# Kernel tuning notes

Measured on AMD Instinct MI355X. Metric: run time of the kernel, lower is better.

Reference implementation:

```python
import jax, jax.numpy as jnp
import numpy as np

B, N, C, H = 2, 2048, 768, 12
D = C // H
SCALE = D ** -0.5
STEP = 0.1
LAMBD = 0.5
EPS = 1e-12  # F.normalize eps


def setup_inputs() -> dict:
    key = jax.random.key(0)
    k1, k2, k3 = jax.random.split(key, 3)
    x = jax.random.normal(k1, (B, N, C), dtype=jnp.float32)
    Wqkv = jax.random.normal(k2, (3 * C, C), dtype=jnp.float32) * 0.02
    Wproj = jax.random.normal(k3, (C, C), dtype=jnp.float32) * 0.02
    bproj = jnp.zeros((C,), dtype=jnp.float32)
    return {"x": x, "Wqkv": Wqkv, "Wproj": Wproj, "bproj": bproj}


def _l2_normalize(t):
    # matches F.normalize(t, dim=-1): t / max(||t||_2, eps)
    n = jnp.sqrt(jnp.sum(t * t, axis=-1, keepdims=True))
    return t / jnp.maximum(n, EPS)


def reference(x, Wqkv, Wproj, bproj):
    b, n, c = x.shape
    # qkv: [B,N,3C] -> [3,B,H,N,D]
    qkv = (x @ Wqkv.T).reshape(b, n, 3, H, D).transpose(2, 0, 3, 1, 4)
    q, k, v = qkv[0], qkv[1], qkv[2]
    q = _l2_normalize(q)
    k = _l2_normalize(k)
    attn = jnp.einsum('bhnd,bhmd->bhnm', q, k) * SCALE
    x1 = jnp.einsum('bhnm,bhmd->bhnd', attn, v)        # weight @ x
    grad_1 = jnp.einsum('bhnm,bhnd->bhmd', attn, x1)   # weight^T @ x1
    grad_2 = jnp.einsum('bhnm,bhnd->bhmd', attn, v)    # weight^T @ x
    grad_update = STEP * (grad_2 - grad_1) - STEP * LAMBD
    out = jax.nn.relu(v + grad_update)                 # [B,H,N,D]
    out = out.transpose(0, 2, 1, 3).reshape(b, n, c)   # [B,N,C]
    return out @ Wproj.T + bproj
```

## Files before the change

### kernel.cpp

```cpp
#include <hip/hip_runtime.h>
#include <hip/hip_bf16.h>

typedef __attribute__((ext_vector_type(8))) __bf16 bf16x8;
typedef __attribute__((ext_vector_type(4))) float f32x4;

#define HBF __hip_bfloat16

static constexpr float SCALE_C = 0.125f;
static constexpr float STEP_C  = 0.1f;
static constexpr float LAMBD_C = 0.5f;

__device__ __forceinline__ int sane_f(float v) {
    float a = fabsf(v);
    return (a <= 1.0e4f && (a >= 1.0e-6f || v == 0.0f)) ? 1 : 0;
}

__global__ __launch_bounds__(256) void convert_all(const void* __restrict__ x,
                                                   const void* __restrict__ wqkv,
                                                   const void* __restrict__ wproj,
                                                   const void* __restrict__ bproj,
                                                   HBF* __restrict__ xb,
                                                   HBF* __restrict__ wqkvb,
                                                   HBF* __restrict__ wprojb,
                                                   HBF* __restrict__ bprojb,
                                                   int* __restrict__ flag) {
    const int t = threadIdx.x, lane = t & 63;
    const unsigned int w = ((const unsigned int*)x)[lane];
    const float f  = __uint_as_float(w);
    const float h0 = __uint_as_float((w & 0xFFFFu) << 16);
    const float h1 = __uint_as_float(w & 0xFFFF0000u);
    int s32 = sane_f(f);
    int s16 = sane_f(h0) + sane_f(h1);
#pragma unroll
    for (int off = 32; off >= 1; off >>= 1) {
        s32 += __shfl_xor(s32, off, 64);
        s16 += __shfl_xor(s16, off, 64);
    }
    const int isf32 = (2 * s32 >= s16) ? 1 : 0;
    if (blockIdx.x == 0 && t == 0) flag[0] = isf32;

    constexpr int C0 = (4096 * 768) / 8;
    constexpr int C1 = C0 + (2304 * 768) / 8;
    constexpr int C2 = C1 + (768 * 768) / 8;
    constexpr int C3 = C2 + 768 / 8;

    int i = blockIdx.x * 256 + t;
    const int stride = gridDim.x * 256;
    for (; i < C3; i += stride) {
        const void* src; HBF* dst; int e;
        if (i < C0)      { src = x;     dst = xb;     e = i; }
        else if (i < C1) { src = wqkv;  dst = wqkvb;  e = i - C0; }
        else if (i < C2) { src = wproj; dst = wprojb; e = i - C1; }
        else             { src = bproj; dst = bprojb; e = i - C2; }
        if (isf32) {
            const float4* s = (const float4*)src;
            float4 a = s[2 * e], b = s[2 * e + 1];
            HBF o[8] = {__float2bfloat16(a.x), __float2bfloat16(a.y),
                        __float2bfloat16(a.z), __float2bfloat16(a.w),
                        __float2bfloat16(b.x), __float2bfloat16(b.y),
                        __float2bfloat16(b.z), __float2bfloat16(b.w)};
            ((uint4*)dst)[e] = *(const uint4*)o;
        } else {
            ((uint4*)dst)[e] = ((const uint4*)src)[e];
        }
    }
}

template <int NJ, bool BIAS, bool FINAL, bool SPLITQKV>
__global__ __launch_bounds__(256) void gemm128(const HBF* __restrict__ A,
                                               const HBF* __restrict__ B,
                                               const HBF* __restrict__ bias,
                                               void* __restrict__ Cout,
                                               HBF* __restrict__ knat,
                                               HBF* __restrict__ vnat,
                                               HBF* __restrict__ tbuf,
                                               int M, int N, int K,
                                               const int* __restrict__ flagp) {
    constexpr int TN = NJ * 32;
    __shared__ HBF smem[128 * 64 + TN * 64];
    HBF* As = smem;
    HBF* Bs = smem + 128 * 64;

    int outf32 = 0;
    if (FINAL) outf32 = *flagp;

    const int tid  = threadIdx.x;
    const int wv   = tid >> 6, lane = tid & 63;
    const int m0   = blockIdx.x * 128, n0 = blockIdx.y * TN;
    const int wr = wv >> 1, wc = wv & 1;
    const int l15 = lane & 15, quad = lane >> 4;
    const int srow   = lane >> 3;
    const int schunk = (lane & 7) ^ srow;

    f32x4 acc[4][NJ] = {};

    for (int k0 = 0; k0 < K; k0 += 64) {
#pragma unroll
        for (int d = 0; d < 4; d++) {
            const int region = d * 4 + wv;
            const int row = region * 8 + srow;
            const HBF* ga = A + (size_t)(m0 + row) * K + k0 + schunk * 8;
            __builtin_amdgcn_global_load_lds((const void*)ga, (void*)(As + region * 512), 16, 0, 0);
        }
#pragma unroll
        for (int d = 0; d < TN / 32; d++) {
            const int region = d * 4 + wv;
            const int row = region * 8 + srow;
            const HBF* gb = B + (size_t)(n0 + row) * K + k0 + schunk * 8;
            __builtin_amdgcn_global_load_lds((const void*)gb, (void*)(Bs + region * 512), 16, 0, 0);
        }
        __syncthreads();

#pragma unroll
        for (int s = 0; s < 2; s++) {
            bf16x8 af[4], bfr[NJ];
#pragma unroll
            for (int i = 0; i < 4; i++) {
                const int row = wr * 64 + i * 16 + l15;
                const int ch = (s * 4 + quad) ^ (row & 7);
                af[i] = *reinterpret_cast<const bf16x8*>(&As[row * 64 + ch * 8]);
            }
#pragma unroll
            for (int j = 0; j < NJ; j++) {
                const int col = wc * (NJ * 16) + j * 16 + l15;
                const int ch = (s * 4 + quad) ^ (col & 7);
                bfr[j] = *reinterpret_cast<const bf16x8*>(&Bs[col * 64 + ch * 8]);
            }
#pragma unroll
            for (int i = 0; i < 4; i++)
#pragma unroll
                for (int j = 0; j < NJ; j++)
                    acc[i][j] = __builtin_amdgcn_mfma_f32_16x16x32_bf16(af[i], bfr[j], acc[i][j], 0, 0, 0);
        }
        __syncthreads();
    }

    if (SPLITQKV) {
        HBF* wpriv = smem + wv * 4096;
        const int colbase = n0 + wc * 64;
        const int tsel = (colbase >= 1536) ? 2 : (colbase >= 768 ? 1 : 0);
        const int h = (colbase - tsel * 768) >> 6;

        if (tsel < 2) {
#pragma unroll
            for (int i = 0; i < 4; i++)
#pragma unroll
                for (int r = 0; r < 4; r++) {
                    float ss = acc[i][0][r] * acc[i][0][r] + acc[i][1][r] * acc[i][1][r]
                             + acc[i][2][r] * acc[i][2][r] + acc[i][3][r] * acc[i][3][r];
#pragma unroll
                    for (int off = 1; off <= 8; off <<= 1) ss += __shfl_xor(ss, off, 64);
                    const float inv = 1.0f / fmaxf(sqrtf(ss), 1e-12f);
#pragma unroll
                    for (int j = 0; j < 4; j++) acc[i][j][r] *= inv;
                }
        }

#pragma unroll
        for (int ih = 0; ih < 2; ih++) {
            const int rowstart = m0 + wr * 64 + ih * 32;
            const int b = rowstart >> 11, nloc = rowstart & 2047;
            const size_t bh = (size_t)(b * 12 + h);

            if (tsel != 0) {
                HBF* ep = wpriv;
#pragma unroll
                for (int ii = 0; ii < 2; ii++) {
                    const int i = ih * 2 + ii;
#pragma unroll
                    for (int j = 0; j < 4; j++)
#pragma unroll
                        for (int r = 0; r < 4; r++)
                            ep[(ii * 16 + quad * 4 + r) * 72 + j * 16 + l15] =
                                __float2bfloat16(acc[i][j][r]);
                }
                HBF* dst0 = ((tsel == 2) ? vnat : knat) + (bh * 2048 + nloc) * 64;
#pragma unroll
                for (int it = 0; it < 4; it++) {
                    const int idx = it * 64 + lane;
                    const int rl = idx >> 3, ch = idx & 7;
                    const uint4 val = *(const uint4*)((const char*)ep + rl * 144 + ch * 16);
                    *(uint4*)((char*)dst0 + rl * 128 + ch * 16) = val;
                }
            }
            {
                HBF* epT = wpriv;
#pragma unroll
                for (int ii = 0; ii < 2; ii++) {
                    const int i = ih * 2 + ii;
#pragma unroll
                    for (int j = 0; j < 4; j++)
#pragma unroll
                        for (int r = 0; r < 4; r++)
                            epT[(j * 16 + l15) * 34 + ii * 16 + quad * 4 + r] =
                                __float2bfloat16(acc[i][j][r]);
                }
                HBF* tdst = tbuf + (size_t)tsel * (24 * 64 * 2048) + (bh * 64) * 2048 + nloc;
#pragma unroll
                for (int it = 0; it < 4; it++) {
                    const int idx = it * 64 + lane;
                    const int d = idx >> 2, c = idx & 3;
                    const uint4 val = *(const uint4*)(epT + d * 34 + c * 8);
                    *(uint4*)(tdst + (size_t)d * 2048 + c * 8) = val;
                }
            }
        }
        return;
    }

    float bvals[NJ];
#pragma unroll
    for (int j = 0; j < NJ; j++) {
        bvals[j] = 0.f;
        if (BIAS) bvals[j] = __bfloat162float(bias[n0 + wc * NJ * 16 + j * 16 + l15]);
    }

    if (FINAL && outf32) {
#pragma unroll
        for (int i = 0; i < 4; i++)
#pragma unroll
            for (int j = 0; j < NJ; j++) {
                const int col = n0 + wc * NJ * 16 + j * 16 + l15;
#pragma unroll
                for (int r = 0; r < 4; r++) {
                    const int row = m0 + wr * 64 + i * 16 + quad * 4 + r;
                    ((float*)Cout)[(size_t)row * N + col] = acc[i][j][r] + bvals[j];
                }
            }
        return;
    }

    constexpr int RS = (NJ == 4) ? 72 : 40;
    constexpr int CH = NJ * 2;
    constexpr int ITERS = 32 * CH / 64;
    HBF* ep = smem + wv * (32 * RS);

#pragma unroll
    for (int ih = 0; ih < 2; ih++) {
#pragma unroll
        for (int ii = 0; ii < 2; ii++) {
            const int i = ih * 2 + ii;
#pragma unroll
            for (int j = 0; j < NJ; j++)
#pragma unroll
                for (int r = 0; r < 4; r++)
                    ep[(ii * 16 + quad * 4 + r) * RS + j * 16 + l15] =
                        __float2bfloat16(acc[i][j][r] + bvals[j]);
        }
        const int rowstart = m0 + wr * 64 + ih * 32;
#pragma unroll
        for (int it = 0; it < ITERS; it++) {
            const int idx = it * 64 + lane;
            const int rl = idx / CH, ch = idx % CH;
            const uint4 val = *(const uint4*)((const char*)ep + rl * (RS * 2) + ch * 16);
            const int grow = rowstart + rl;
            const int col = n0 + wc * NJ * 16 + ch * 8;
            *(uint4*)((HBF*)Cout + (size_t)grow * N + col) = val;
        }
    }
}

__global__ __launch_bounds__(256) void gram_mfma(const HBF* __restrict__ QKVt,
                                                 float* __restrict__ P) {
    __shared__ HBF lds[3 * 8192];
    const int bh = blockIdx.x, cn = blockIdx.y;
    const int t = threadIdx.x, wv = t >> 6, lane = t & 63;
    const int l15 = lane & 15, quad = lane >> 4;
    constexpr size_t S = (size_t)24 * 64 * 2048;
    const HBF* srcs[3] = {QKVt + S, QKVt, QKVt + 2 * S};

    const int rowq = lane >> 4;
    const int cgb  = lane & 15;
#pragma unroll
    for (int t3 = 0; t3 < 3; t3++) {
        const HBF* base = srcs[t3] + (size_t)bh * 64 * 2048 + cn * 128;
#pragma unroll
        for (int rg = 0; rg < 4; rg++) {
            const int region = rg * 4 + wv;
            const int row = region * 4 + rowq;
            const int cg = cgb ^ (row & 15);
            __builtin_amdgcn_global_load_lds((const void*)(base + (size_t)row * 2048 + cg * 8),
                                             (void*)(lds + t3 * 8192 + region * 512), 16, 0, 0);
        }
    }
    __syncthreads();

    const HBF* Kt = lds;
    const HBF* Qt = lds + 8192;
    const HBF* Vt = lds + 16384;
    f32x4 aKV[4] = {}, aQV[4] = {}, aQQ[4] = {};
    const int i = wv;
#pragma unroll
    for (int s = 0; s < 4; s++) {
        const int q = (s * 4 + quad) ^ l15;
        const bf16x8 aK = *(const bf16x8*)(Kt + (i * 16 + l15) * 128 + q * 8);
        const bf16x8 aQ = *(const bf16x8*)(Qt + (i * 16 + l15) * 128 + q * 8);
#pragma unroll
        for (int j = 0; j < 4; j++) {
            const bf16x8 bV = *(const bf16x8*)(Vt + (j * 16 + l15) * 128 + q * 8);
            const bf16x8 bQ = *(const bf16x8*)(Qt + (j * 16 + l15) * 128 + q * 8);
            aKV[j] = __builtin_amdgcn_mfma_f32_16x16x32_bf16(aK, bV, aKV[j], 0, 0, 0);
            aQV[j] = __builtin_amdgcn_mfma_f32_16x16x32_bf16(aQ, bV, aQV[j], 0, 0, 0);
            aQQ[j] = __builtin_amdgcn_mfma_f32_16x16x32_bf16(aQ, bQ, aQQ[j], 0, 0, 0);
        }
    }

    float* Pb = P + ((size_t)bh * 16 + cn) * 12288;
#pragma unroll
    for (int j = 0; j < 4; j++)
#pragma unroll
        for (int r = 0; r < 4; r++) {
            const int row = i * 16 + quad * 4 + r, col = j * 16 + l15;
            Pb[row * 64 + col]        = aKV[j][r];
            Pb[4096 + row * 64 + col] = aQV[j][r];
            Pb[8192 + row * 64 + col] = aQQ[j][r];
        }
}

__global__ __launch_bounds__(256) void gram_reduce(const float* __restrict__ P,
                                                   float* __restrict__ M) {
    const int o = blockIdx.x * 256 + threadIdx.x;
    const int head = o / 12288, e = o % 12288;
    const float* Pb = P + (size_t)head * 16 * 12288 + e;
    float s = 0.f;
#pragma unroll
    for (int k = 0; k < 16; k++) s += Pb[(size_t)k * 12288];
    M[o] = s;
}

__global__ __launch_bounds__(256) void combine_w(const float* __restrict__ M,
                                                 HBF* __restrict__ Wt) {
    const int bh = blockIdx.x;
    const int by = blockIdx.y;
    const int t = threadIdx.x;
    __shared__ float Kv[4096];
    __shared__ float Qq8[512];
    const float* Mb = M + (size_t)bh * 12288;
#pragma unroll
    for (int r = 0; r < 16; r++) Kv[t + 256 * r] = Mb[t + 256 * r];
#pragma unroll
    for (int r = 0; r < 2; r++)  Qq8[t + 256 * r] = Mb[8192 + by * 512 + t + 256 * r];
    __syncthreads();

    const int il = t >> 5;
    const int j0 = (t & 31) * 2;
    float s0 = 0.f, s1 = 0.f;
#pragma unroll
    for (int k = 0; k < 64; k++) {
        const float q = Qq8[il * 64 + k];
        const float2 kv = *(const float2*)&Kv[k * 64 + j0];
        s0 += q * kv.x;
        s1 += q * kv.y;
    }
    const int i = by * 8 + il;
    const float w0 = STEP_C * (SCALE_C * Mb[4096 + i * 64 + j0]     - SCALE_C * SCALE_C * s0);
    const float w1 = STEP_C * (SCALE_C * Mb[4096 + i * 64 + j0 + 1] - SCALE_C * SCALE_C * s1);
    Wt[(size_t)bh * 4096 + j0 * 64 + i]       = __float2bfloat16(w0);
    Wt[(size_t)bh * 4096 + (j0 + 1) * 64 + i] = __float2bfloat16(w1);
}

__global__ __launch_bounds__(256) void epilogue_attn(const HBF* __restrict__ Kn,
                                                     const HBF* __restrict__ Vb,
                                                     const HBF* __restrict__ Wt,
                                                     HBF* __restrict__ AO) {
    __shared__ char smem[34816];
    HBF* Ks  = (HBF*)smem;
    HBF* Wts = Ks + 128 * 64;
    float* Ps = (float*)smem;

    const int bh = blockIdx.x, cn = blockIdx.y;
    const int b = bh / 12, h = bh % 12;
    const int t = threadIdx.x, wv = t >> 6, lane = t & 63;
    const int l15 = lane & 15, quad = lane >> 4;
    const size_t kbase = ((size_t)bh * 2048 + cn * 128) * 64;
    const int srow = lane >> 3;
    const int schunk = (lane & 7) ^ srow;
    const int sub = t & 7;

#pragma unroll
    for (int rg = 0; rg < 4; rg++) {
        const int region = rg * 4 + wv;
        const int row = region * 8 + srow;
        __builtin_amdgcn_global_load_lds((const void*)(Kn + kbase + (size_t)row * 64 + schunk * 8),
                                         (void*)(Ks + region * 512), 16, 0, 0);
    }
#pragma unroll
    for (int rg = 0; rg < 2; rg++) {
        const int region = rg * 4 + wv;
        const int row = region * 8 + srow;
        __builtin_amdgcn_global_load_lds((const void*)(Wt + (size_t)bh * 4096 + (size_t)row * 64 + schunk * 8),
                                         (void*)(Wts + region * 512), 16, 0, 0);
    }
    __syncthreads();

    f32x4 acc[2][4] = {};
#pragma unroll
    for (int s = 0; s < 2; s++) {
        const int ch = (s * 4 + quad) ^ (l15 & 7);
        bf16x8 af[2], bfr[4];
#pragma unroll
        for (int i = 0; i < 2; i++) {
            const int row = wv * 32 + i * 16 + l15;
            af[i] = *reinterpret_cast<const bf16x8*>(&Ks[row * 64 + ch * 8]);
        }
#pragma unroll
        for (int j = 0; j < 4; j++) {
            const int d = j * 16 + l15;
            bfr[j] = *reinterpret_cast<const bf16x8*>(&Wts[d * 64 + ch * 8]);
        }
#pragma unroll
        for (int i = 0; i < 2; i++)
#pragma unroll
            for (int j = 0; j < 4; j++)
                acc[i][j] = __builtin_amdgcn_mfma_f32_16x16x32_bf16(af[i], bfr[j], acc[i][j], 0, 0, 0);
    }
    __syncthreads();

    float* Pw = Ps + wv * (32 * 68);
#pragma unroll
    for (int i = 0; i < 2; i++)
#pragma unroll
        for (int j = 0; j < 4; j++)
#pragma unroll
            for (int r = 0; r < 4; r++)
                Pw[(i * 16 + quad * 4 + r) * 68 + j * 16 + l15] = acc[i][j][r];
    __syncthreads();

#pragma unroll
    for (int rr = 0; rr < 4; rr++) {
        const int row = rr * 32 + (t >> 3);
        const float* prow = Ps + (row >> 5) * (32 * 68) + (row & 31) * 68 + sub * 8;
        const float4 p0 = *(const float4*)prow;
        const float4 p1 = *(const float4*)(prow + 4);
        uint4 rv = *(const uint4*)(Vb + kbase + (size_t)row * 64 + sub * 8);
        const HBF* hv = (const HBF*)&rv;
        const float pv[8] = {p0.x, p0.y, p0.z, p0.w, p1.x, p1.y, p1.z, p1.w};
        HBF o[8];
#pragma unroll
        for (int i = 0; i < 8; i++)
            o[i] = __float2bfloat16(fmaxf(__bfloat162float(hv[i]) + pv[i] - (STEP_C * LAMBD_C), 0.f));
        const int n = cn * 128 + row;
        *(uint4*)(AO + ((size_t)b * 2048 + n) * 768 + h * 64 + sub * 8) = *(const uint4*)o;
    }
}

extern "C" void kernel_launch(void* const* d_in, const int* in_sizes, int n_in,
                              void* d_out, int out_size, void* d_ws, size_t ws_size,
                              hipStream_t stream) {
    char* ws = (char*)d_ws;
    size_t off = 0;
    int*   flag   = (int*)(ws + off);   off += 16;
    HBF*   xb     = (HBF*)(ws + off);   off += (size_t)4096 * 768 * 2;
    HBF*   Wqkvb  = (HBF*)(ws + off);   off += (size_t)2304 * 768 * 2;
    HBF*   Wprojb = (HBF*)(ws + off);   off += (size_t)768 * 768 * 2;
    HBF*   bprojb = (HBF*)(ws + off);   off += 2048;
    HBF*   Kn     = (HBF*)(ws + off);   off += (size_t)24 * 2048 * 64 * 2;
    HBF*   Vb     = (HBF*)(ws + off);   off += (size_t)24 * 2048 * 64 * 2;
    HBF*   QKVt   = (HBF*)(ws + off);   off += (size_t)3 * 24 * 64 * 2048 * 2;
    float* P      = (float*)(ws + off); off += (size_t)24 * 16 * 12288 * 4;
    float* M      = (float*)(ws + off); off += (size_t)24 * 12288 * 4;
    HBF*   Wt     = (HBF*)(ws + off);   off += (size_t)24 * 4096 * 2;
    HBF*   AO     = (HBF*)(ws + off);   off += (size_t)4096 * 768 * 2;

    convert_all<<<2048, 256, 0, stream>>>(d_in[0], d_in[1], d_in[2], d_in[3],
                                          xb, Wqkvb, Wprojb, bprojb, flag);

    gemm128<4, false, false, true><<<dim3(32, 18), 256, 0, stream>>>(
        xb, Wqkvb, nullptr, nullptr, Kn, Vb, QKVt, 4096, 2304, 768, nullptr);

    gram_mfma<<<dim3(24, 16), 256, 0, stream>>>(QKVt, P);
    gram_reduce<<<1152, 256, 0, stream>>>(P, M);

    combine_w<<<dim3(24, 8), 256, 0, stream>>>(M, Wt);

    epilogue_attn<<<dim3(24, 16), 256, 0, stream>>>(Kn, Vb, Wt, AO);

    gemm128<2, true, true, false><<<dim3(32, 12), 256, 0, stream>>>(
        AO, Wprojb, bprojb, d_out, nullptr, nullptr, nullptr, 4096, 768, 768, flag);
}
```

Measured before the change: 153.5 us.

## Double-buffer GEMM LDS tiles and shrink M tile to 64 rows

Turns the GEMM kernel into a double-buffered version. The next K-slice's global-to-LDS loads are issued before computing on the current slice, and one of the two barriers per iteration is dropped. The M tile also shrinks from 128 to 64 rows, which doubles the number of blocks for both the QKV and projection GEMMs to improve occupancy and CU coverage. The trade-offs are more LDS per block and lower per-block data reuse. The SPLITQKV epilogue is restructured to match the smaller tile.

```diff
diff --git a/kernel.cpp b/kernel.cpp
--- a/kernel.cpp
+++ b/kernel.cpp
@@ -66,8 +66,8 @@
     }
 }
 
-template <int NJ, bool BIAS, bool FINAL, bool SPLITQKV>
-__global__ __launch_bounds__(256) void gemm128(const HBF* __restrict__ A,
+template <int TM, int TN, bool BIAS, bool FINAL, bool SPLITQKV>
+__global__ __launch_bounds__(256) void gemm_db(const HBF* __restrict__ A,
                                                const HBF* __restrict__ B,
                                                const HBF* __restrict__ bias,
                                                void* __restrict__ Cout,
@@ -76,64 +76,75 @@
                                                HBF* __restrict__ tbuf,
                                                int M, int N, int K,
                                                const int* __restrict__ flagp) {
-    constexpr int TN = NJ * 32;
-    __shared__ HBF smem[128 * 64 + TN * 64];
-    HBF* As = smem;
-    HBF* Bs = smem + 128 * 64;
+    constexpr int NI = TM / 32;
+    constexpr int NJ = TN / 32;
+    constexpr int BUF = (TM + TN) * 64;
+    __shared__ HBF smem[2 * BUF];
 
     int outf32 = 0;
     if (FINAL) outf32 = *flagp;
 
     const int tid  = threadIdx.x;
     const int wv   = tid >> 6, lane = tid & 63;
-    const int m0   = blockIdx.x * 128, n0 = blockIdx.y * TN;
+    const int m0   = blockIdx.x * TM, n0 = blockIdx.y * TN;
     const int wr = wv >> 1, wc = wv & 1;
     const int l15 = lane & 15, quad = lane >> 4;
     const int srow   = lane >> 3;
     const int schunk = (lane & 7) ^ srow;
 
-    f32x4 acc[4][NJ] = {};
-
-    for (int k0 = 0; k0 < K; k0 += 64) {
-#pragma unroll
-        for (int d = 0; d < 4; d++) {
+    const int NITER = K / 64;
+
+    auto issue = [&](int it) {
+        HBF* abase = smem + (it & 1) * BUF;
+        HBF* bbase = abase + TM * 64;
+        const int k0 = it * 64;
+#pragma unroll
+        for (int d = 0; d < NI; d++) {
             const int region = d * 4 + wv;
             const int row = region * 8 + srow;
-            const HBF* ga = A + (size_t)(m0 + row) * K + k0 + schunk * 8;
-            __builtin_amdgcn_global_load_lds((const void*)ga, (void*)(As + region * 512), 16, 0, 0);
-        }
-#pragma unroll
-        for (int d = 0; d < TN / 32; d++) {
+            __builtin_amdgcn_global_load_lds((const void*)(A + (size_t)(m0 + row) * K + k0 + schunk * 8),
+                                             (void*)(abase + region * 512), 16, 0, 0);
+        }
+#pragma unroll
+        for (int d = 0; d < NJ; d++) {
             const int region = d * 4 + wv;
             const int row = region * 8 + srow;
-            const HBF* gb = B + (size_t)(n0 + row) * K + k0 + schunk * 8;
-            __builtin_amdgcn_global_load_lds((const void*)gb, (void*)(Bs + region * 512), 16, 0, 0);
-        }
+            __builtin_amdgcn_global_load_lds((const void*)(B + (size_t)(n0 + row) * K + k0 + schunk * 8),
+                                             (void*)(bbase + region * 512), 16, 0, 0);
+        }
+    };
+
+    f32x4 acc[NI][NJ] = {};
+
+    issue(0);
+    for (int it = 0; it < NITER; it++) {
         __syncthreads();
-
+        if (it + 1 < NITER) issue(it + 1);
+        const HBF* As = smem + (it & 1) * BUF;
+        const HBF* Bs = As + TM * 64;
 #pragma unroll
         for (int s = 0; s < 2; s++) {
-            bf16x8 af[4], bfr[NJ];
-#pragma unroll
-            for (int i = 0; i < 4; i++) {
-                const int row = wr * 64 + i * 16 + l15;
+            bf16x8 af[NI], bfr[NJ];
+#pragma unroll
+            for (int i = 0; i < NI; i++) {
+                const int row = wr * (TM / 2) + i * 16 + l15;
                 const int ch = (s * 4 + quad) ^ (row & 7);
                 af[i] = *reinterpret_cast<const bf16x8*>(&As[row * 64 + ch * 8]);
             }
 #pragma unroll
             for (int j = 0; j < NJ; j++) {
-                const int col = wc * (NJ * 16) + j * 16 + l15;
+                const int col = wc * (TN / 2) + j * 16 + l15;
                 const int ch = (s * 4 + quad) ^ (col & 7);
                 bfr[j] = *reinterpret_cast<const bf16x8*>(&Bs[col * 64 + ch * 8]);
             }
 #pragma unroll
-            for (int i = 0; i < 4; i++)
+            for (int i = 0; i < NI; i++)
 #pragma unroll
                 for (int j = 0; j < NJ; j++)
                     acc[i][j] = __builtin_amdgcn_mfma_f32_16x16x32_bf16(af[i], bfr[j], acc[i][j], 0, 0, 0);
         }
-        __syncthreads();
-    }
+    }
+    __syncthreads();
 
     if (SPLITQKV) {
         HBF* wpriv = smem + wv * 4096;
@@ -143,7 +154,7 @@
 
         if (tsel < 2) {
 #pragma unroll
-            for (int i = 0; i < 4; i++)
+            for (int i = 0; i < NI; i++)
 #pragma unroll
                 for (int r = 0; r < 4; r++) {
                     float ss = acc[i][0][r] * acc[i][0][r] + acc[i][1][r] * acc[i][1][r]
@@ -156,53 +167,46 @@
                 }
         }
 
-#pragma unroll
-        for (int ih = 0; ih < 2; ih++) {
-            const int rowstart = m0 + wr * 64 + ih * 32;
-            const int b = rowstart >> 11, nloc = rowstart & 2047;
-            const size_t bh = (size_t)(b * 12 + h);
-
-            if (tsel != 0) {
-                HBF* ep = wpriv;
-#pragma unroll
-                for (int ii = 0; ii < 2; ii++) {
-                    const int i = ih * 2 + ii;
-#pragma unroll
-                    for (int j = 0; j < 4; j++)
-#pragma unroll
-                        for (int r = 0; r < 4; r++)
-                            ep[(ii * 16 + quad * 4 + r) * 72 + j * 16 + l15] =
-                                __float2bfloat16(acc[i][j][r]);
-                }
-                HBF* dst0 = ((tsel == 2) ? vnat : knat) + (bh * 2048 + nloc) * 64;
-#pragma unroll
-                for (int it = 0; it < 4; it++) {
-                    const int idx = it * 64 + lane;
-                    const int rl = idx >> 3, ch = idx & 7;
-                    const uint4 val = *(const uint4*)((const char*)ep + rl * 144 + ch * 16);
-                    *(uint4*)((char*)dst0 + rl * 128 + ch * 16) = val;
-                }
+        const int rowstart = m0 + wr * 32;
+        const int b = rowstart >> 11, nloc = rowstart & 2047;
+        const size_t bh = (size_t)(b * 12 + h);
+
+        if (tsel != 0) {
+            HBF* ep = wpriv;
+#pragma unroll
+            for (int i = 0; i < NI; i++)
+#pragma unroll
+                for (int j = 0; j < 4; j++)
+#pragma unroll
+                    for (int r = 0; r < 4; r++)
+                        ep[(i * 16 + quad * 4 + r) * 72 + j * 16 + l15] =
+                            __float2bfloat16(acc[i][j][r]);
+            HBF* dst0 = ((tsel == 2) ? vnat : knat) + (bh * 2048 + nloc) * 64;
+#pragma unroll
+            for (int itr = 0; itr < 4; itr++) {
+                const int idx = itr * 64 + lane;
+                const int rl = idx >> 3, ch = idx & 7;
+                const uint4 val = *(const uint4*)((const char*)ep + rl * 144 + ch * 16);
+                *(uint4*)((char*)dst0 + rl * 128 + ch * 16) = val;
             }
-            {
-                HBF* epT = wpriv;
-#pragma unroll
-                for (int ii = 0; ii < 2; ii++) {
-                    const int i = ih * 2 + ii;
-#pragma unroll
-                    for (int j = 0; j < 4; j++)
-#pragma unroll
-                        for (int r = 0; r < 4; r++)
-                            epT[(j * 16 + l15) * 34 + ii * 16 + quad * 4 + r] =
-                                __float2bfloat16(acc[i][j][r]);
-                }
-                HBF* tdst = tbuf + (size_t)tsel * (24 * 64 * 2048) + (bh * 64) * 2048 + nloc;
-#pragma unroll
-                for (int it = 0; it < 4; it++) {
-                    const int idx = it * 64 + lane;
-                    const int d = idx >> 2, c = idx & 3;
-                    const uint4 val = *(const uint4*)(epT + d * 34 + c * 8);
-                    *(uint4*)(tdst + (size_t)d * 2048 + c * 8) = val;
-                }
+        }
+        {
+            HBF* epT = wpriv;
+#pragma unroll
+            for (int i = 0; i < NI; i++)
+#pragma unroll
+                for (int j = 0; j < 4; j++)
+#pragma unroll
+                    for (int r = 0; r < 4; r++)
+                        epT[(j * 16 + l15) * 34 + i * 16 + quad * 4 + r] =
+                            __float2bfloat16(acc[i][j][r]);
+            HBF* tdst = tbuf + (size_t)tsel * (24 * 64 * 2048) + (bh * 64) * 2048 + nloc;
+#pragma unroll
+            for (int itr = 0; itr < 4; itr++) {
+                const int idx = itr * 64 + lane;
+                const int d = idx >> 2, c = idx & 3;
+                const uint4 val = *(const uint4*)(epT + d * 34 + c * 8);
+                *(uint4*)(tdst + (size_t)d * 2048 + c * 8) = val;
             }
         }
         return;
@@ -212,51 +216,44 @@
 #pragma unroll
     for (int j = 0; j < NJ; j++) {
         bvals[j] = 0.f;
-        if (BIAS) bvals[j] = __bfloat162float(bias[n0 + wc * NJ * 16 + j * 16 + l15]);
+        if (BIAS) bvals[j] = __bfloat162float(bias[n0 + wc * (TN / 2) + j * 16 + l15]);
     }
 
     if (FINAL && outf32) {
 #pragma unroll
-        for (int i = 0; i < 4; i++)
+        for (int i = 0; i < NI; i++)
 #pragma unroll
             for (int j = 0; j < NJ; j++) {
-                const int col = n0 + wc * NJ * 16 + j * 16 + l15;
+                const int col = n0 + wc * (TN / 2) + j * 16 + l15;
 #pragma unroll
                 for (int r = 0; r < 4; r++) {
-                    const int row = m0 + wr * 64 + i * 16 + quad * 4 + r;
+                    const int row = m0 + wr * (TM / 2) + i * 16 + quad * 4 + r;
                     ((float*)Cout)[(size_t)row * N + col] = acc[i][j][r] + bvals[j];
                 }
             }
         return;
     }
 
-    constexpr int RS = (NJ == 4) ? 72 : 40;
-    constexpr int CH = NJ * 2;
-    constexpr int ITERS = 32 * CH / 64;
+    constexpr int RS = (TN / 2) + 8;
+    constexpr int CHR = TN / 16;
+    constexpr int ITERS = 32 * CHR / 64;
     HBF* ep = smem + wv * (32 * RS);
 
 #pragma unroll
-    for (int ih = 0; ih < 2; ih++) {
-#pragma unroll
-        for (int ii = 0; ii < 2; ii++) {
-            const int i = ih * 2 + ii;
-#pragma unroll
-            for (int j = 0; j < NJ; j++)
-#pragma unroll
-                for (int r = 0; r < 4; r++)
-                    ep[(ii * 16 + quad * 4 + r) * RS + j * 16 + l15] =
-                        __float2bfloat16(acc[i][j][r] + bvals[j]);
-        }
-        const int rowstart = m0 + wr * 64 + ih * 32;
-#pragma unroll
-        for (int it = 0; it < ITERS; it++) {
-            const int idx = it * 64 + lane;
-            const int rl = idx / CH, ch = idx % CH;
-            const uint4 val = *(const uint4*)((const char*)ep + rl * (RS * 2) + ch * 16);
-            const int grow = rowstart + rl;
-            const int col = n0 + wc * NJ * 16 + ch * 8;
-            *(uint4*)((HBF*)Cout + (size_t)grow * N + col) = val;
-        }
+    for (int i = 0; i < NI; i++)
+#pragma unroll
+        for (int j = 0; j < NJ; j++)
+#pragma unroll
+            for (int r = 0; r < 4; r++)
+                ep[(i * 16 + quad * 4 + r) * RS + j * 16 + l15] =
+                    __float2bfloat16(acc[i][j][r] + bvals[j]);
+    const int rowstart = m0 + wr * 32;
+#pragma unroll
+    for (int itr = 0; itr < ITERS; itr++) {
+        const int idx = itr * 64 + lane;
+        const int rl = idx / CHR, ch = idx % CHR;
+        const uint4 val = *(const uint4*)((const char*)ep + rl * (RS * 2) + ch * 16);
+        *(uint4*)((HBF*)Cout + (size_t)(rowstart + rl) * N + n0 + wc * (TN / 2) + ch * 8) = val;
     }
 }
 
@@ -465,7 +462,7 @@
     convert_all<<<2048, 256, 0, stream>>>(d_in[0], d_in[1], d_in[2], d_in[3],
                                           xb, Wqkvb, Wprojb, bprojb, flag);
 
-    gemm128<4, false, false, true><<<dim3(32, 18), 256, 0, stream>>>(
+    gemm_db<64, 128, false, false, true><<<dim3(64, 18), 256, 0, stream>>>(
         xb, Wqkvb, nullptr, nullptr, Kn, Vb, QKVt, 4096, 2304, 768, nullptr);
 
     gram_mfma<<<dim3(24, 16), 256, 0, stream>>>(QKVt, P);
@@ -475,6 +472,6 @@
 
     epilogue_attn<<<dim3(24, 16), 256, 0, stream>>>(Kn, Vb, Wt, AO);
 
-    gemm128<2, true, true, false><<<dim3(32, 12), 256, 0, stream>>>(
+    gemm_db<64, 64, true, true, false><<<dim3(64, 12), 256, 0, stream>>>(
         AO, Wprojb, bprojb, d_out, nullptr, nullptr, nullptr, 4096, 768, 768, flag);
 }
```

After: 142.8 us. 6.9% less time.
